# Kernel tuning notes

Hardware: AMD Instinct MI355X
Metric: run time of the kernel (lower is better)

The kernel has to match this reference:

```python
import jax, jax.numpy as jnp
import numpy as np

EPS = 1e-5  # torch LayerNorm default

def layer_norm(x, scale, bias):
    m = jnp.mean(x, axis=-1, keepdims=True)
    v = jnp.var(x, axis=-1, keepdims=True)
    return (x - m) * jax.lax.rsqrt(v + EPS) * scale + bias

def setup_inputs() -> dict:
    key = jax.random.key(0)
    ks = jax.random.split(key, 8)
    B, N, E, D = 2, 50000, 262144, 256
    node_features = jax.random.normal(ks[0], (B, N, D), jnp.float32)
    edge_index = jax.random.randint(ks[1], (B, E, 2), 0, N)
    edge_relations = jax.random.normal(ks[2], (B, E, D), jnp.float32)
    edge_mask = jnp.ones((B, E), jnp.float32)
    sc = 1.0 / np.sqrt(D).astype(np.float32)
    rel_w = jax.random.normal(ks[3], (D, D), jnp.float32) * sc
    rel_b = jnp.zeros((D,), jnp.float32)
    norm_s = jnp.ones((D,), jnp.float32)
    norm_b = jnp.zeros((D,), jnp.float32)
    w1 = jax.random.normal(ks[4], (D, 4 * D), jnp.float32) * sc
    b1 = jnp.zeros((4 * D,), jnp.float32)
    w2 = jax.random.normal(ks[5], (4 * D, D), jnp.float32) * (1.0 / np.sqrt(4 * D).astype(np.float32))
    b2 = jnp.zeros((D,), jnp.float32)
    ffn_s = jnp.ones((D,), jnp.float32)
    ffn_b = jnp.zeros((D,), jnp.float32)
    return dict(node_features=node_features, edge_relations=edge_relations,
                edge_mask=edge_mask, rel_w=rel_w, rel_b=rel_b,
                norm_s=norm_s, norm_b=norm_b, w1=w1, b1=b1, w2=w2, b2=b2,
                ffn_s=ffn_s, ffn_b=ffn_b, edge_index=edge_index)

def reference(node_features, edge_relations, edge_mask, rel_w, rel_b,
              norm_s, norm_b, w1, b1, w2, b2, ffn_s, ffn_b, edge_index):
    B, N, D = node_features.shape
    bidx = jnp.arange(B)[:, None]                      # [B,1] batch index for gather/scatter
    src_idx = edge_index[:, :, 0]                      # [B,E]
    tgt_idx = edge_index[:, :, 1]                      # [B,E]
    src_features = node_features[bidx, src_idx]        # gather -> [B,E,D]
    rel_features = edge_relations @ rel_w + rel_b      # [B,E,D]
    messages = (src_features + rel_features) * edge_mask[..., None]
    aggregated = jnp.zeros_like(node_features).at[bidx, tgt_idx].add(messages)
    counts = jnp.zeros((B, N, 1), node_features.dtype).at[bidx, tgt_idx].add(edge_mask[..., None])
    counts = jnp.maximum(counts, 1.0)
    aggregated = aggregated / counts
    x = layer_norm(node_features + aggregated, norm_s, norm_b)
    h = jax.nn.gelu(x @ w1 + b1, approximate=False)    # torch GELU default = exact erf
    x = layer_norm(x + (h @ w2 + b2), ffn_s, ffn_b)
    return x
```

## Files before the change

kernel.cpp:

```cpp
#include <hip/hip_runtime.h>
#include <math.h>

#define Bn 2
#define Nn 50000
#define En 262144
#define Dn 256
#define Hn 1024
#define RTOT (Bn*Nn)

typedef short bf16x8 __attribute__((ext_vector_type(8)));
typedef float f32x4 __attribute__((ext_vector_type(4)));

__device__ __forceinline__ short f2b(float f) {
  unsigned u = __float_as_uint(f);
  u = u + 0x7fffu + ((u >> 16) & 1u);
  return (short)(u >> 16);
}
__device__ __forceinline__ float b2f(unsigned short s) {
  return __uint_as_float(((unsigned)s) << 16);
}

__device__ __forceinline__ float gelu_f(float v) {
  float x = fabsf(v) * 0.70710678118654752f;
  float t = __builtin_amdgcn_rcpf(1.0f + 0.47047f * x);
  float p = t*(0.3480242f + t*(-0.0958798f + t*0.7478556f));
  float er = 1.0f - p * __expf(-x*x);
  er = copysignf(er, v);
  return 0.5f * v * (1.0f + er);
}

__device__ __forceinline__ void gl16(const void* g, void* l) {
  __builtin_amdgcn_global_load_lds(
      (const __attribute__((address_space(1))) unsigned int*)g,
      (__attribute__((address_space(3))) unsigned int*)l, 16, 0, 0);
}

__global__ void __launch_bounds__(256) wconv(
    const float* __restrict__ relw, const float* __restrict__ w1,
    const float* __restrict__ w2, short* __restrict__ relwT,
    short* __restrict__ w1s, short* __restrict__ w2s) {
  int tid = blockIdx.x * 256 + threadIdx.x;
  if (tid < Dn*Dn) { int c = tid >> 8, k = tid & 255; relwT[tid] = f2b(relw[k*Dn + c]); }
  int t1 = tid - Dn*Dn;
  if (t1 >= 0 && t1 < Dn*Hn) {
    int kk = t1 >> 16, rem = t1 & 65535;
    int col = rem >> 6, kl = rem & 63;
    w1s[kk*65536 + col*64 + (kl ^ ((col & 7) << 3))] = f2b(w1[(kk*64 + kl)*Hn + col]);
  }
  int t2 = tid - Dn*Dn - Dn*Hn;
  if (t2 >= 0 && t2 < Hn*Dn) {
    int kk = t2 >> 14, rem = t2 & 16383;
    int col = rem >> 6, kl = rem & 63;
    w2s[kk*16384 + col*64 + (kl ^ ((col & 7) << 3))] = f2b(w2[(kk*64 + kl)*Dn + col]);
  }
}

__global__ void __launch_bounds__(256) histk(const int* __restrict__ ei, int* __restrict__ cnt) {
  int tid = blockIdx.x * 256 + threadIdx.x;
  if (tid >= Bn*En) return;
  int b = tid / En;
  int tgt = ei[tid*2 + 1];
  atomicAdd(&cnt[b*Nn + tgt], 1);
}

__global__ void __launch_bounds__(256) offsk(const int* __restrict__ cnt,
                                             int* __restrict__ offs, int* __restrict__ gtot) {
  int i = blockIdx.x * 256 + threadIdx.x;
  int lane = threadIdx.x & 63;
  int v = (i < RTOT) ? cnt[i] : 0;
  int s = v;
#pragma unroll
  for (int d = 1; d < 64; d <<= 1) {
    int t = __shfl_up(s, d, 64);
    if (lane >= d) s += t;
  }
  int base = 0;
  if (lane == 63) base = atomicAdd(gtot, s);
  base = __shfl(base, 63, 64);
  if (i < RTOT) offs[i] = base + s - v;
}

__global__ void __launch_bounds__(256) fillk(const int* __restrict__ ei, const int* __restrict__ offs,
                                             int* __restrict__ cursor, int* __restrict__ eids) {
  int tid = blockIdx.x * 256 + threadIdx.x;
  if (tid >= Bn*En) return;
  int b = tid / En, e = tid - b*En;
  int tgt = ei[tid*2 + 1];
  int node = b*Nn + tgt;
  int pos = atomicAdd(&cursor[node], 1);
  eids[offs[node] + pos] = e;
}

__global__ void __launch_bounds__(256) aggk(
    const float* __restrict__ nodef, const float* __restrict__ erel,
    const float* __restrict__ emask, const int* __restrict__ ei,
    const int* __restrict__ offs, const int* __restrict__ cnt,
    const int* __restrict__ eids,
    short* __restrict__ sumrelB, short* __restrict__ sumsrcB, float* __restrict__ cntf) {
  int w = (blockIdx.x * 256 + threadIdx.x) >> 6;
  int lane = threadIdx.x & 63;
  if (w >= RTOT) return;
  int b = w / Nn;
  const size_t ebase = (size_t)b * En;
  const size_t nbase = (size_t)b * Nn;
  int s0 = offs[w], kall = cnt[w];
  int h = lane >> 5, l32 = lane & 31;
  float r[8] = {}, a[8] = {};
  float cf = 0.f;
  for (int base = 0; base < kall; base += 64) {
    int k = kall - base; if (k > 64) k = 64;
    int e = 0, sr = 0; float m = 0.f;
    if (lane < k) {
      e  = eids[s0 + base + lane];
      sr = ei[(ebase + e)*2];
      m  = emask[ebase + e];
    }
    for (int j = 0; j < k; j += 2) {
      int je = j + h;
      int e1  = __shfl(e, je, 64);
      int sr1 = __shfl(sr, je, 64);
      float m1 = __shfl(m, je, 64);
      if (je < k) {
        const float* rp = erel  + (ebase + e1)*Dn + l32*8;
        const float* np = nodef + (nbase + sr1)*Dn + l32*8;
        float4 rv0 = *(const float4*)rp;
        float4 rv1 = *(const float4*)(rp + 4);
        float4 nv0 = *(const float4*)np;
        float4 nv1 = *(const float4*)(np + 4);
        r[0]+=rv0.x*m1; r[1]+=rv0.y*m1; r[2]+=rv0.z*m1; r[3]+=rv0.w*m1;
        r[4]+=rv1.x*m1; r[5]+=rv1.y*m1; r[6]+=rv1.z*m1; r[7]+=rv1.w*m1;
        a[0]+=nv0.x*m1; a[1]+=nv0.y*m1; a[2]+=nv0.z*m1; a[3]+=nv0.w*m1;
        a[4]+=nv1.x*m1; a[5]+=nv1.y*m1; a[6]+=nv1.z*m1; a[7]+=nv1.w*m1;
        cf += m1;
      }
    }
  }
#pragma unroll
  for (int i = 0; i < 8; i++) {
    r[i] += __shfl_xor(r[i], 32, 64);
    a[i] += __shfl_xor(a[i], 32, 64);
  }
  cf += __shfl_xor(cf, 32, 64);
  bf16x8 o;
  if (h == 0) {
#pragma unroll
    for (int i = 0; i < 8; i++) o[i] = f2b(r[i]);
    *(bf16x8*)((char*)sumrelB + (size_t)w*512 + ((l32*16) ^ ((w & 7) << 4))) = o;
  } else {
#pragma unroll
    for (int i = 0; i < 8; i++) o[i] = f2b(a[i]);
    *(bf16x8*)((char*)sumsrcB + (size_t)w*512 + l32*16) = o;
  }
  if (lane == 0) cntf[w] = cf;
}

__device__ __forceinline__ bf16x8 ldsA(const char* lds, int r, int kb) {
  int byte = r*512 + (((kb)*2) ^ ((r & 7) << 4));
  return *(const bf16x8*)(lds + byte);
}

__global__ void __launch_bounds__(256, 4) relln(
    const short* __restrict__ sumrelB, const short* __restrict__ relwT,
    const float* __restrict__ relb, const float* __restrict__ nodef,
    const short* __restrict__ sumsrcB, const float* __restrict__ cntf,
    const float* __restrict__ ns, const float* __restrict__ nb,
    short* __restrict__ xb) {
  constexpr int MR = 2;
  __shared__ __align__(16) char lds[16384 + 1024];
  float* red = (float*)(lds + 16384);
  int tid = threadIdx.x;
  int lane = tid & 63, wv = tid >> 6;
  int l15 = lane & 15, l4 = lane >> 4;
  int row0 = blockIdx.x * 32;
#pragma unroll
  for (int i = 0; i < 4; i++) {
    int u = tid + 256*i;
    int r = u >> 5, wb = (u & 31) * 16;
    gl16((const char*)sumrelB + (size_t)(row0 + r)*512 + wb, lds + u*16);
  }
  __syncthreads();
  f32x4 acc[MR][4] = {};
#pragma unroll
  for (int ks = 0; ks < 8; ks++) {
    bf16x8 af[MR], bfr[4];
#pragma unroll
    for (int m = 0; m < MR; m++) af[m] = ldsA(lds, m*16 + l15, ks*32 + l4*8);
#pragma unroll
    for (int n = 0; n < 4; n++) {
      int col = wv*64 + n*16 + l15;
      bfr[n] = *(const bf16x8*)(relwT + col*Dn + ks*32 + l4*8);
    }
#pragma unroll
    for (int m = 0; m < MR; m++)
#pragma unroll
      for (int n = 0; n < 4; n++)
        acc[m][n] = __builtin_amdgcn_mfma_f32_16x16x32_bf16(af[m], bfr[n], acc[m][n], 0, 0, 0);
  }
  int cols[4]; float rb_c[4], ns_c[4], nb_c[4];
#pragma unroll
  for (int n = 0; n < 4; n++) {
    cols[n] = wv*64 + n*16 + l15;
    rb_c[n] = relb[cols[n]]; ns_c[n] = ns[cols[n]]; nb_c[n] = nb[cols[n]];
  }
  float s1[MR][4], s2[MR][4];
#pragma unroll
  for (int m = 0; m < MR; m++)
#pragma unroll
    for (int g = 0; g < 4; g++) {
      int r = m*16 + l4*4 + g; int rg = row0 + r;
      float cf  = cntf[rg];
      float inv = 1.0f / fmaxf(cf, 1.0f);
      float aa = 0.f, qq = 0.f;
#pragma unroll
      for (int n = 0; n < 4; n++) {
        float ssrc = b2f(*(const unsigned short*)((const char*)sumsrcB + (size_t)rg*512 + cols[n]*2));
        float nfv  = nodef[(size_t)rg*Dn + cols[n]];
        float vv = nfv + (ssrc + acc[m][n][g] + cf*rb_c[n]) * inv;
        acc[m][n][g] = vv;
        aa += vv; qq += vv*vv;
      }
#pragma unroll
      for (int d = 1; d < 16; d <<= 1) { aa += __shfl_xor(aa, d, 16); qq += __shfl_xor(qq, d, 16); }
      s1[m][g] = aa; s2[m][g] = qq;
    }
  if (l15 == 0) {
#pragma unroll
    for (int m = 0; m < MR; m++)
#pragma unroll
      for (int g = 0; g < 4; g++) {
        int r = m*16 + l4*4 + g;
        red[(wv*32 + r)*2]     = s1[m][g];
        red[(wv*32 + r)*2 + 1] = s2[m][g];
      }
  }
  __syncthreads();
#pragma unroll
  for (int m = 0; m < MR; m++)
#pragma unroll
    for (int g = 0; g < 4; g++) {
      int r = m*16 + l4*4 + g; int rg = row0 + r;
      float t1 = 0.f, t2 = 0.f;
#pragma unroll
      for (int u = 0; u < 4; u++) { t1 += red[(u*32 + r)*2]; t2 += red[(u*32 + r)*2 + 1]; }
      float mean = t1 * (1.0f/Dn);
      float var  = t2 * (1.0f/Dn) - mean*mean;
      float rstd = rsqrtf(var + 1e-5f);
#pragma unroll
      for (int n = 0; n < 4; n++) {
        float xv = (acc[m][n][g] - mean)*rstd*ns_c[n] + nb_c[n];
        *(short*)((char*)xb + (size_t)rg*512 + ((cols[n]*2) ^ ((rg & 7) << 4))) = f2b(xv);
      }
    }
}

__global__ void __launch_bounds__(256) ffn1k(
    const short* __restrict__ xb, const short* __restrict__ w1s,
    const float* __restrict__ b1, short* __restrict__ H) {
  __shared__ __align__(16) char lds[32768];
  char* Xa = lds;
  char* Wa = lds + 16384;
  int tid = threadIdx.x;
  int lane = tid & 63, wv = tid >> 6;
  int l15 = lane & 15, l4 = lane >> 4;
  int wm = wv >> 1, wn = wv & 1;
  int row0 = blockIdx.x * 128;
  int col0 = blockIdx.y * 128;

  f32x4 acc[4][4] = {};
#pragma unroll 1
  for (int kk = 0; kk < 4; kk++) {
#pragma unroll
    for (int i = 0; i < 4; i++) {
      int u = tid + 256*i;
      int r = u >> 3, wb = (u & 7) * 16;
      int gr = row0 + r; if (gr > RTOT - 1) gr = RTOT - 1;
      gl16((const char*)xb + (size_t)gr*512 + kk*128 + wb, Xa + u*16);
    }
#pragma unroll
    for (int i = 0; i < 4; i++) {
      int u = tid + 256*i;
      gl16((const char*)w1s + (size_t)kk*131072 + col0*128 + u*16, Wa + u*16);
    }
    __syncthreads();
#pragma unroll
    for (int ksl = 0; ksl < 2; ksl++) {
      int kb2 = (ksl*32 + l4*8) * 2;
      bf16x8 af[4], bw[4];
#pragma unroll
      for (int mf = 0; mf < 4; mf++) {
        int r = wm*64 + mf*16 + l15;
        af[mf] = *(const bf16x8*)(Xa + r*128 + (kb2 ^ ((r & 7) << 4)));
      }
#pragma unroll
      for (int nf = 0; nf < 4; nf++) {
        int c = wn*64 + nf*16 + l15;
        bw[nf] = *(const bf16x8*)(Wa + c*128 + (kb2 ^ ((c & 7) << 4)));
      }
#pragma unroll
      for (int mf = 0; mf < 4; mf++)
#pragma unroll
        for (int nf = 0; nf < 4; nf++)
          acc[mf][nf] = __builtin_amdgcn_mfma_f32_16x16x32_bf16(af[mf], bw[nf], acc[mf][nf], 0, 0, 0);
    }
    __syncthreads();
  }
  float b1v[4];
#pragma unroll
  for (int nf = 0; nf < 4; nf++) b1v[nf] = b1[col0 + wn*64 + nf*16 + l15];
#pragma unroll
  for (int mf = 0; mf < 4; mf++)
#pragma unroll
    for (int g = 0; g < 4; g++) {
      int R = wm*64 + mf*16 + l4*4 + g;
#pragma unroll
      for (int nf = 0; nf < 4; nf++) {
        int C = wn*64 + nf*16 + l15;
        float hv = gelu_f(acc[mf][nf][g] + b1v[nf]);
        *(short*)(lds + R*256 + ((C*2) ^ ((R & 7) << 4))) = f2b(hv);
      }
    }
  __syncthreads();
#pragma unroll
  for (int i = 0; i < 8; i++) {
    int u = tid + 256*i;
    int r = u >> 4, c = (u & 15) * 8;
    int gr = row0 + r;
    if (gr >= RTOT) continue;
    bf16x8 v = *(const bf16x8*)(lds + r*256 + ((c*2) ^ ((r & 7) << 4)));
    int gc = col0 + c;
    size_t hb = (size_t)gr*2048 + (gc >> 6)*128 + (((gc & 63)*2) ^ ((gr & 7) << 4));
    *(bf16x8*)((char*)H + hb) = v;
  }
}

__global__ void __launch_bounds__(512, 4) ffn2k(
    const short* __restrict__ H, const short* __restrict__ w2s,
    const float* __restrict__ b2, const float* __restrict__ fs,
    const float* __restrict__ fb, const short* __restrict__ xb,
    float* __restrict__ out) {
  __shared__ __align__(16) char lds[8192 + 32768];
  char* Ha  = lds;
  char* W2a = lds + 8192;
  float* red = (float*)lds;
  int tid = threadIdx.x;
  int lane = tid & 63, wv = tid >> 6;
  int l15 = lane & 15, l4 = lane >> 4;
  int wm = wv >> 2, wn = wv & 3;
  int rows0 = blockIdx.x * 64;

  f32x4 acc[2][4] = {};
#pragma unroll 1
  for (int kk = 0; kk < 16; kk++) {
    {
      int flat = wv*1024 + lane*16;
      int r = flat >> 7, bo = flat & 127;
      int lr = rows0 + r; if (lr > RTOT - 1) lr = RTOT - 1;
      gl16((const char*)H + (size_t)lr*2048 + kk*128 + bo, Ha + flat);
    }
#pragma unroll
    for (int i = 0; i < 4; i++) {
      int base = wv*4096 + i*1024;
      gl16((const char*)w2s + (size_t)kk*32768 + base + lane*16, W2a + base + lane*16);
    }
    __syncthreads();
#pragma unroll
    for (int ksl = 0; ksl < 2; ksl++) {
      bf16x8 ah[2], bw[4];
#pragma unroll
      for (int mf = 0; mf < 2; mf++) {
        int r = wm*32 + mf*16 + l15;
        ah[mf] = *(const bf16x8*)(Ha + r*128 + (((ksl*32 + l4*8)*2) ^ ((r & 7) << 4)));
      }
#pragma unroll
      for (int nf = 0; nf < 4; nf++) {
        int c = wn*64 + nf*16 + l15;
        bw[nf] = *(const bf16x8*)(W2a + c*128 + (((ksl*32 + l4*8)*2) ^ ((c & 7) << 4)));
      }
#pragma unroll
      for (int mf = 0; mf < 2; mf++)
#pragma unroll
        for (int nf = 0; nf < 4; nf++)
          acc[mf][nf] = __builtin_amdgcn_mfma_f32_16x16x32_bf16(ah[mf], bw[nf], acc[mf][nf], 0, 0, 0);
    }
    __syncthreads();
  }
  float b2c[4], fsc[4], fbc[4];
#pragma unroll
  for (int nf = 0; nf < 4; nf++) {
    int col = wn*64 + nf*16 + l15;
    b2c[nf] = b2[col]; fsc[nf] = fs[col]; fbc[nf] = fb[col];
  }
#pragma unroll
  for (int mf = 0; mf < 2; mf++)
#pragma unroll
    for (int g = 0; g < 4; g++) {
      int R = wm*32 + mf*16 + l4*4 + g;
      int gr = rows0 + R;
      bool ok = gr < RTOT;
      float a = 0.f, q = 0.f;
#pragma unroll
      for (int nf = 0; nf < 4; nf++) {
        int col = wn*64 + nf*16 + l15;
        float xv = 0.f;
        if (ok) xv = b2f(*(const unsigned short*)((const char*)xb + (size_t)gr*512 + ((col*2) ^ ((gr & 7) << 4))));
        float vv = xv + acc[mf][nf][g] + b2c[nf];
        acc[mf][nf][g] = vv;
        a += vv; q += vv*vv;
      }
#pragma unroll
      for (int d = 1; d < 16; d <<= 1) { a += __shfl_xor(a, d, 16); q += __shfl_xor(q, d, 16); }
      if (l15 == 0) {
        red[(wn*64 + R)*2]     = a;
        red[(wn*64 + R)*2 + 1] = q;
      }
    }
  __syncthreads();
#pragma unroll
  for (int mf = 0; mf < 2; mf++)
#pragma unroll
    for (int g = 0; g < 4; g++) {
      int R = wm*32 + mf*16 + l4*4 + g;
      int gr = rows0 + R;
      if (gr >= RTOT) continue;
      float t1 = 0.f, t2 = 0.f;
#pragma unroll
      for (int u = 0; u < 4; u++) { t1 += red[(u*64 + R)*2]; t2 += red[(u*64 + R)*2 + 1]; }
      float mean = t1 * (1.0f/Dn);
      float var  = t2 * (1.0f/Dn) - mean*mean;
      float rstd = rsqrtf(var + 1e-5f);
#pragma unroll
      for (int nf = 0; nf < 4; nf++) {
        int col = wn*64 + nf*16 + l15;
        out[(size_t)gr*Dn + col] = (acc[mf][nf][g] - mean)*rstd*fsc[nf] + fbc[nf];
      }
    }
}

extern "C" void kernel_launch(void* const* d_in, const int* in_sizes, int n_in,
                              void* d_out, int out_size, void* d_ws, size_t ws_size,
                              hipStream_t stream) {
  const float* nodef = (const float*)d_in[0];
  const float* erel  = (const float*)d_in[1];
  const float* emask = (const float*)d_in[2];
  const float* relw  = (const float*)d_in[3];
  const float* relb  = (const float*)d_in[4];
  const float* ns    = (const float*)d_in[5];
  const float* nb    = (const float*)d_in[6];
  const float* w1    = (const float*)d_in[7];
  const float* b1    = (const float*)d_in[8];
  const float* w2    = (const float*)d_in[9];
  const float* b2    = (const float*)d_in[10];
  const float* fs    = (const float*)d_in[11];
  const float* fb    = (const float*)d_in[12];
  const int*   ei    = (const int*)d_in[13];
  float* out = (float*)d_out;
  char* ws = (char*)d_ws;

  constexpr size_t SZ_ROWB = (size_t)RTOT * Dn * 2;
  constexpr size_t O_SRB = 0;
  constexpr size_t O_SSB = O_SRB + SZ_ROWB;
  constexpr size_t O_XB  = O_SSB + SZ_ROWB;
  constexpr size_t O_H   = O_XB + SZ_ROWB;
  constexpr size_t O_CNT = O_H + (size_t)RTOT * Hn * 2;
  constexpr size_t O_CUR = O_CNT + (size_t)RTOT*4;
  constexpr size_t O_OFF = O_CUR + (size_t)RTOT*4;
  constexpr size_t O_EID = O_OFF + ((size_t)(RTOT+1)*4 + 124);
  constexpr size_t O_CNTF = O_EID + (size_t)Bn*En*4;
  constexpr size_t O_RWT = O_CNTF + (size_t)RTOT*4;
  constexpr size_t O_W1T = O_RWT + (size_t)Dn*Dn*2;
  constexpr size_t O_W2T = O_W1T + (size_t)Dn*Hn*2;
  constexpr size_t WS_NEED = O_W2T + (size_t)Hn*Dn*2;
  if (ws_size < WS_NEED) return;

  short* sumrelB = (short*)(ws + O_SRB);
  short* sumsrcB = (short*)(ws + O_SSB);
  short* xb      = (short*)(ws + O_XB);
  short* Hbuf    = (short*)(ws + O_H);
  int*   cnt    = (int*)(ws + O_CNT);
  int*   cursor = (int*)(ws + O_CUR);
  int*   offs   = (int*)(ws + O_OFF);
  int*   eids   = (int*)(ws + O_EID);
  float* cntf   = (float*)(ws + O_CNTF);
  short* relwT  = (short*)(ws + O_RWT);
  short* w1s    = (short*)(ws + O_W1T);
  short* w2s    = (short*)(ws + O_W2T);
  int*   gtot   = offs + RTOT;

  hipMemsetAsync(ws + O_CNT, 0, O_EID - O_CNT, stream);

  wconv<<<(Dn*Dn + Dn*Hn + Hn*Dn + 255) / 256, 256, 0, stream>>>(relw, w1, w2, relwT, w1s, w2s);
  histk<<<(Bn*En) / 256, 256, 0, stream>>>(ei, cnt);
  offsk<<<(RTOT + 255) / 256, 256, 0, stream>>>(cnt, offs, gtot);
  fillk<<<(Bn*En) / 256, 256, 0, stream>>>(ei, offs, cursor, eids);
  aggk<<<(RTOT + 3) / 4, 256, 0, stream>>>(nodef, erel, emask, ei, offs, cnt, eids,
                                           sumrelB, sumsrcB, cntf);
  relln<<<RTOT / 32, 256, 0, stream>>>(sumrelB, relwT, relb, nodef, sumsrcB, cntf, ns, nb, xb);
  ffn1k<<<dim3((RTOT + 127) / 128, Hn / 128), 256, 0, stream>>>(xb, w1s, b1, Hbuf);
  ffn2k<<<(RTOT + 63) / 64, 512, 0, stream>>>(Hbuf, w2s, b2, fs, fb, xb, out);
}
```

Before: 633.2 us.

## Pack edge records in CSR fill and widen ffn2 row tile to 128

```diff
diff --git a/kernel.cpp b/kernel.cpp
--- a/kernel.cpp
+++ b/kernel.cpp
@@ -80,22 +80,23 @@
   if (i < RTOT) offs[i] = base + s - v;
 }
 
-__global__ void __launch_bounds__(256) fillk(const int* __restrict__ ei, const int* __restrict__ offs,
-                                             int* __restrict__ cursor, int* __restrict__ eids) {
+__global__ void __launch_bounds__(256) fillk(const int* __restrict__ ei,
+                                             const float* __restrict__ emask,
+                                             int* __restrict__ offs, int4* __restrict__ erec) {
   int tid = blockIdx.x * 256 + threadIdx.x;
   if (tid >= Bn*En) return;
   int b = tid / En, e = tid - b*En;
-  int tgt = ei[tid*2 + 1];
-  int node = b*Nn + tgt;
-  int pos = atomicAdd(&cursor[node], 1);
-  eids[offs[node] + pos] = e;
+  int2 st = *(const int2*)(ei + (size_t)tid*2);
+  float m = emask[tid];
+  int node = b*Nn + st.y;
+  int pos = atomicAdd(&offs[node], 1);
+  erec[pos] = make_int4(e, st.x, __float_as_int(m), 0);
 }
 
 __global__ void __launch_bounds__(256) aggk(
     const float* __restrict__ nodef, const float* __restrict__ erel,
-    const float* __restrict__ emask, const int* __restrict__ ei,
     const int* __restrict__ offs, const int* __restrict__ cnt,
-    const int* __restrict__ eids,
+    const int4* __restrict__ erec,
     short* __restrict__ sumrelB, short* __restrict__ sumsrcB, float* __restrict__ cntf) {
   int w = (blockIdx.x * 256 + threadIdx.x) >> 6;
   int lane = threadIdx.x & 63;
@@ -103,23 +104,20 @@
   int b = w / Nn;
   const size_t ebase = (size_t)b * En;
   const size_t nbase = (size_t)b * Nn;
-  int s0 = offs[w], kall = cnt[w];
+  int kall = cnt[w];
+  int s0 = offs[w] - kall;
   int h = lane >> 5, l32 = lane & 31;
   float r[8] = {}, a[8] = {};
   float cf = 0.f;
   for (int base = 0; base < kall; base += 64) {
     int k = kall - base; if (k > 64) k = 64;
-    int e = 0, sr = 0; float m = 0.f;
-    if (lane < k) {
-      e  = eids[s0 + base + lane];
-      sr = ei[(ebase + e)*2];
-      m  = emask[ebase + e];
-    }
+    int4 rec = make_int4(0, 0, 0, 0);
+    if (lane < k) rec = erec[s0 + base + lane];
     for (int j = 0; j < k; j += 2) {
       int je = j + h;
-      int e1  = __shfl(e, je, 64);
-      int sr1 = __shfl(sr, je, 64);
-      float m1 = __shfl(m, je, 64);
+      int e1  = __shfl(rec.x, je, 64);
+      int sr1 = __shfl(rec.y, je, 64);
+      float m1 = __int_as_float(__shfl(rec.z, je, 64));
       if (je < k) {
         const float* rp = erel  + (ebase + e1)*Dn + l32*8;
         const float* np = nodef + (nbase + sr1)*Dn + l32*8;
@@ -338,46 +336,41 @@
     const float* __restrict__ b2, const float* __restrict__ fs,
     const float* __restrict__ fb, const short* __restrict__ xb,
     float* __restrict__ out) {
-  __shared__ __align__(16) char lds[8192 + 32768];
+  __shared__ __align__(16) char lds[16384 + 4096];
   char* Ha  = lds;
-  char* W2a = lds + 8192;
-  float* red = (float*)lds;
+  float* red = (float*)(lds + 16384);
   int tid = threadIdx.x;
   int lane = tid & 63, wv = tid >> 6;
   int l15 = lane & 15, l4 = lane >> 4;
   int wm = wv >> 2, wn = wv & 3;
-  int rows0 = blockIdx.x * 64;
-
-  f32x4 acc[2][4] = {};
+  int rows0 = blockIdx.x * 128;
+
+  f32x4 acc[4][4] = {};
 #pragma unroll 1
   for (int kk = 0; kk < 16; kk++) {
-    {
-      int flat = wv*1024 + lane*16;
+#pragma unroll
+    for (int i = 0; i < 2; i++) {
+      int flat = (wv*2 + i)*1024 + lane*16;
       int r = flat >> 7, bo = flat & 127;
       int lr = rows0 + r; if (lr > RTOT - 1) lr = RTOT - 1;
       gl16((const char*)H + (size_t)lr*2048 + kk*128 + bo, Ha + flat);
     }
-#pragma unroll
-    for (int i = 0; i < 4; i++) {
-      int base = wv*4096 + i*1024;
-      gl16((const char*)w2s + (size_t)kk*32768 + base + lane*16, W2a + base + lane*16);
-    }
     __syncthreads();
 #pragma unroll
     for (int ksl = 0; ksl < 2; ksl++) {
-      bf16x8 ah[2], bw[4];
-#pragma unroll
-      for (int mf = 0; mf < 2; mf++) {
-        int r = wm*32 + mf*16 + l15;
+      bf16x8 ah[4], bw[4];
+#pragma unroll
+      for (int mf = 0; mf < 4; mf++) {
+        int r = wm*64 + mf*16 + l15;
         ah[mf] = *(const bf16x8*)(Ha + r*128 + (((ksl*32 + l4*8)*2) ^ ((r & 7) << 4)));
       }
 #pragma unroll
       for (int nf = 0; nf < 4; nf++) {
         int c = wn*64 + nf*16 + l15;
-        bw[nf] = *(const bf16x8*)(W2a + c*128 + (((ksl*32 + l4*8)*2) ^ ((c & 7) << 4)));
-      }
-#pragma unroll
-      for (int mf = 0; mf < 2; mf++)
+        bw[nf] = *(const bf16x8*)(w2s + kk*16384 + c*64 + ((ksl*32 + l4*8) ^ ((c & 7) << 3)));
+      }
+#pragma unroll
+      for (int mf = 0; mf < 4; mf++)
 #pragma unroll
         for (int nf = 0; nf < 4; nf++)
           acc[mf][nf] = __builtin_amdgcn_mfma_f32_16x16x32_bf16(ah[mf], bw[nf], acc[mf][nf], 0, 0, 0);
@@ -391,10 +384,10 @@
     b2c[nf] = b2[col]; fsc[nf] = fs[col]; fbc[nf] = fb[col];
   }
 #pragma unroll
-  for (int mf = 0; mf < 2; mf++)
+  for (int mf = 0; mf < 4; mf++)
 #pragma unroll
     for (int g = 0; g < 4; g++) {
-      int R = wm*32 + mf*16 + l4*4 + g;
+      int R = wm*64 + mf*16 + l4*4 + g;
       int gr = rows0 + R;
       bool ok = gr < RTOT;
       float a = 0.f, q = 0.f;
@@ -410,21 +403,21 @@
 #pragma unroll
       for (int d = 1; d < 16; d <<= 1) { a += __shfl_xor(a, d, 16); q += __shfl_xor(q, d, 16); }
       if (l15 == 0) {
-        red[(wn*64 + R)*2]     = a;
-        red[(wn*64 + R)*2 + 1] = q;
+        red[(wn*128 + R)*2]     = a;
+        red[(wn*128 + R)*2 + 1] = q;
       }
     }
   __syncthreads();
 #pragma unroll
-  for (int mf = 0; mf < 2; mf++)
+  for (int mf = 0; mf < 4; mf++)
 #pragma unroll
     for (int g = 0; g < 4; g++) {
-      int R = wm*32 + mf*16 + l4*4 + g;
+      int R = wm*64 + mf*16 + l4*4 + g;
       int gr = rows0 + R;
       if (gr >= RTOT) continue;
       float t1 = 0.f, t2 = 0.f;
 #pragma unroll
-      for (int u = 0; u < 4; u++) { t1 += red[(u*64 + R)*2]; t2 += red[(u*64 + R)*2 + 1]; }
+      for (int u = 0; u < 4; u++) { t1 += red[(u*128 + R)*2]; t2 += red[(u*128 + R)*2 + 1]; }
       float mean = t1 * (1.0f/Dn);
       float var  = t2 * (1.0f/Dn) - mean*mean;
       float rstd = rsqrtf(var + 1e-5f);
@@ -462,10 +455,10 @@
   constexpr size_t O_XB  = O_SSB + SZ_ROWB;
   constexpr size_t O_H   = O_XB + SZ_ROWB;
   constexpr size_t O_CNT = O_H + (size_t)RTOT * Hn * 2;
-  constexpr size_t O_CUR = O_CNT + (size_t)RTOT*4;
-  constexpr size_t O_OFF = O_CUR + (size_t)RTOT*4;
-  constexpr size_t O_EID = O_OFF + ((size_t)(RTOT+1)*4 + 124);
-  constexpr size_t O_CNTF = O_EID + (size_t)Bn*En*4;
+  constexpr size_t O_GT  = O_CNT + (size_t)RTOT*4;
+  constexpr size_t O_OFF = O_GT + 128;
+  constexpr size_t O_REC = O_OFF + (size_t)RTOT*4 + 112;
+  constexpr size_t O_CNTF = O_REC + (size_t)Bn*En*16;
   constexpr size_t O_RWT = O_CNTF + (size_t)RTOT*4;
   constexpr size_t O_W1T = O_RWT + (size_t)Dn*Dn*2;
   constexpr size_t O_W2T = O_W1T + (size_t)Dn*Hn*2;
@@ -477,24 +470,23 @@
   short* xb      = (short*)(ws + O_XB);
   short* Hbuf    = (short*)(ws + O_H);
   int*   cnt    = (int*)(ws + O_CNT);
-  int*   cursor = (int*)(ws + O_CUR);
+  int*   gtot   = (int*)(ws + O_GT);
   int*   offs   = (int*)(ws + O_OFF);
-  int*   eids   = (int*)(ws + O_EID);
+  int4*  erec   = (int4*)(ws + O_REC);
   float* cntf   = (float*)(ws + O_CNTF);
   short* relwT  = (short*)(ws + O_RWT);
   short* w1s    = (short*)(ws + O_W1T);
   short* w2s    = (short*)(ws + O_W2T);
-  int*   gtot   = offs + RTOT;
-
-  hipMemsetAsync(ws + O_CNT, 0, O_EID - O_CNT, stream);
+
+  hipMemsetAsync(ws + O_CNT, 0, (size_t)RTOT*4 + 128, stream);
 
   wconv<<<(Dn*Dn + Dn*Hn + Hn*Dn + 255) / 256, 256, 0, stream>>>(relw, w1, w2, relwT, w1s, w2s);
   histk<<<(Bn*En) / 256, 256, 0, stream>>>(ei, cnt);
   offsk<<<(RTOT + 255) / 256, 256, 0, stream>>>(cnt, offs, gtot);
-  fillk<<<(Bn*En) / 256, 256, 0, stream>>>(ei, offs, cursor, eids);
-  aggk<<<(RTOT + 3) / 4, 256, 0, stream>>>(nodef, erel, emask, ei, offs, cnt, eids,
+  fillk<<<(Bn*En) / 256, 256, 0, stream>>>(ei, emask, offs, erec);
+  aggk<<<(RTOT + 3) / 4, 256, 0, stream>>>(nodef, erel, offs, cnt, erec,
                                            sumrelB, sumsrcB, cntf);
   relln<<<RTOT / 32, 256, 0, stream>>>(sumrelB, relwT, relb, nodef, sumsrcB, cntf, ns, nb, xb);
   ffn1k<<<dim3((RTOT + 127) / 128, Hn / 128), 256, 0, stream>>>(xb, w1s, b1, Hbuf);
-  ffn2k<<<(RTOT + 63) / 64, 512, 0, stream>>>(Hbuf, w2s, b2, fs, fb, xb, out);
-}
+  ffn2k<<<(RTOT + 127) / 128, 512, 0, stream>>>(Hbuf, w2s, b2, fs, fb, xb, out);
+}
```

After: 676.2 us. +6.8%, slower.

## Stage epilogue residual inputs through LDS with coalesced loads

Applied to the files above, without the earlier changes.

```diff
diff --git a/kernel.cpp b/kernel.cpp
--- a/kernel.cpp
+++ b/kernel.cpp
@@ -149,7 +149,7 @@
   } else {
 #pragma unroll
     for (int i = 0; i < 8; i++) o[i] = f2b(a[i]);
-    *(bf16x8*)((char*)sumsrcB + (size_t)w*512 + l32*16) = o;
+    *(bf16x8*)((char*)sumsrcB + (size_t)w*512 + ((l32*16) ^ ((w & 7) << 4))) = o;
   }
   if (lane == 0) cntf[w] = cf;
 }
@@ -159,15 +159,17 @@
   return *(const bf16x8*)(lds + byte);
 }
 
-__global__ void __launch_bounds__(256, 4) relln(
+__global__ void __launch_bounds__(256, 3) relln(
     const short* __restrict__ sumrelB, const short* __restrict__ relwT,
     const float* __restrict__ relb, const float* __restrict__ nodef,
     const short* __restrict__ sumsrcB, const float* __restrict__ cntf,
     const float* __restrict__ ns, const float* __restrict__ nb,
     short* __restrict__ xb) {
   constexpr int MR = 2;
-  __shared__ __align__(16) char lds[16384 + 1024];
-  float* red = (float*)(lds + 16384);
+  __shared__ __align__(16) char lds[16384 + 33280 + 1024];
+  char* ldsS = lds;
+  char* ldsN = lds + 16384;
+  float* red = (float*)(lds + 16384 + 33280);
   int tid = threadIdx.x;
   int lane = tid & 63, wv = tid >> 6;
   int l15 = lane & 15, l4 = lane >> 4;
@@ -176,7 +178,14 @@
   for (int i = 0; i < 4; i++) {
     int u = tid + 256*i;
     int r = u >> 5, wb = (u & 31) * 16;
-    gl16((const char*)sumrelB + (size_t)(row0 + r)*512 + wb, lds + u*16);
+    gl16((const char*)sumrelB + (size_t)(row0 + r)*512 + wb, ldsS + u*16);
+  }
+#pragma unroll
+  for (int i = 0; i < 8; i++) {
+    int u = tid + 256*i;
+    int r = u >> 6, c4 = u & 63;
+    float4 v = *(const float4*)(nodef + (size_t)(row0 + r)*Dn + c4*4);
+    *(float4*)(ldsN + r*1040 + c4*16) = v;
   }
   __syncthreads();
   f32x4 acc[MR][4] = {};
@@ -184,7 +193,7 @@
   for (int ks = 0; ks < 8; ks++) {
     bf16x8 af[MR], bfr[4];
 #pragma unroll
-    for (int m = 0; m < MR; m++) af[m] = ldsA(lds, m*16 + l15, ks*32 + l4*8);
+    for (int m = 0; m < MR; m++) af[m] = ldsA(ldsS, m*16 + l15, ks*32 + l4*8);
 #pragma unroll
     for (int n = 0; n < 4; n++) {
       int col = wv*64 + n*16 + l15;
@@ -196,6 +205,14 @@
       for (int n = 0; n < 4; n++)
         acc[m][n] = __builtin_amdgcn_mfma_f32_16x16x32_bf16(af[m], bfr[n], acc[m][n], 0, 0, 0);
   }
+  __syncthreads();
+#pragma unroll
+  for (int i = 0; i < 4; i++) {
+    int u = tid + 256*i;
+    int r = u >> 5, wb = (u & 31) * 16;
+    gl16((const char*)sumsrcB + (size_t)(row0 + r)*512 + wb, ldsS + u*16);
+  }
+  __syncthreads();
   int cols[4]; float rb_c[4], ns_c[4], nb_c[4];
 #pragma unroll
   for (int n = 0; n < 4; n++) {
@@ -213,8 +230,8 @@
       float aa = 0.f, qq = 0.f;
 #pragma unroll
       for (int n = 0; n < 4; n++) {
-        float ssrc = b2f(*(const unsigned short*)((const char*)sumsrcB + (size_t)rg*512 + cols[n]*2));
-        float nfv  = nodef[(size_t)rg*Dn + cols[n]];
+        float ssrc = b2f(*(const unsigned short*)(ldsS + r*512 + ((cols[n]*2) ^ ((r & 7) << 4))));
+        float nfv  = *(const float*)(ldsN + r*1040 + cols[n]*4);
         float vv = nfv + (ssrc + acc[m][n][g] + cf*rb_c[n]) * inv;
         acc[m][n][g] = vv;
         aa += vv; qq += vv*vv;
@@ -384,6 +401,14 @@
     }
     __syncthreads();
   }
+#pragma unroll
+  for (int i = 0; i < 4; i++) {
+    int u = tid + 512*i;
+    int r = u >> 5, wb = (u & 31) * 16;
+    int lr = rows0 + r; if (lr > RTOT - 1) lr = RTOT - 1;
+    gl16((const char*)xb + (size_t)lr*512 + wb, W2a + u*16);
+  }
+  __syncthreads();
   float b2c[4], fsc[4], fbc[4];
 #pragma unroll
   for (int nf = 0; nf < 4; nf++) {
@@ -395,14 +420,11 @@
 #pragma unroll
     for (int g = 0; g < 4; g++) {
       int R = wm*32 + mf*16 + l4*4 + g;
-      int gr = rows0 + R;
-      bool ok = gr < RTOT;
       float a = 0.f, q = 0.f;
 #pragma unroll
       for (int nf = 0; nf < 4; nf++) {
         int col = wn*64 + nf*16 + l15;
-        float xv = 0.f;
-        if (ok) xv = b2f(*(const unsigned short*)((const char*)xb + (size_t)gr*512 + ((col*2) ^ ((gr & 7) << 4))));
+        float xv = b2f(*(const unsigned short*)(W2a + R*512 + ((col*2) ^ ((R & 7) << 4))));
         float vv = xv + acc[mf][nf][g] + b2c[nf];
         acc[mf][nf][g] = vv;
         a += vv; q += vv*vv;
```

Result: faster. 612.1 us (-3.3%).
